# Kernel tuning notes

Measured on AMD Instinct MI355X. Metric: run time of the kernel, lower is better.

The kernel has to match this reference:

```python
import jax, jax.numpy as jnp
import numpy as np

N_LAYERS = 6
C = 768          # hidden_channels
FC = 3072        # filter_channels
H = 12           # n_heads
KC = C // H      # k_channels = 64
KS = 3           # ffn kernel_size
W = 4            # window_size
B = 8
T = 512
EPS = 1e-5


def setup_inputs() -> dict:
    key = jax.random.key(0)
    ks = iter(jax.random.split(key, 24))
    def rn(shape, s=0.02):
        return jax.random.normal(next(ks), shape, dtype=jnp.float32) * s
    inp = {}
    inp['x'] = jax.random.normal(next(ks), (B, C, T), dtype=jnp.float32)
    inp['x_lengths'] = jax.random.randint(next(ks), (B,), T // 2, T + 1, dtype=jnp.int32)
    inp['conv_q_w'] = rn((N_LAYERS, C, C))
    inp['conv_q_b'] = rn((N_LAYERS, C))
    inp['conv_k_w'] = rn((N_LAYERS, C, C))
    inp['conv_k_b'] = rn((N_LAYERS, C))
    inp['conv_v_w'] = rn((N_LAYERS, C, C))
    inp['conv_v_b'] = rn((N_LAYERS, C))
    inp['conv_o_w'] = rn((N_LAYERS, C, C))
    inp['conv_o_b'] = rn((N_LAYERS, C))
    inp['emb_rel_k'] = rn((N_LAYERS, 1, 2 * W + 1, KC), KC ** -0.5)
    inp['emb_rel_v'] = rn((N_LAYERS, 1, 2 * W + 1, KC), KC ** -0.5)
    inp['norm1_g'] = jnp.ones((N_LAYERS, C), jnp.float32)
    inp['norm1_b'] = jnp.zeros((N_LAYERS, C), jnp.float32)
    inp['ffn_w1'] = rn((N_LAYERS, FC, C, KS))
    inp['ffn_b1'] = rn((N_LAYERS, FC))
    inp['ffn_w2'] = rn((N_LAYERS, C, FC, KS))
    inp['ffn_b2'] = rn((N_LAYERS, C))
    inp['norm2_g'] = jnp.ones((N_LAYERS, C), jnp.float32)
    inp['norm2_b'] = jnp.zeros((N_LAYERS, C), jnp.float32)
    return inp


def _layer_norm(x, g, b):
    # x: [B, C, T]; normalize over channel dim (torch code transposes then layer_norms)
    m = jnp.mean(x, axis=1, keepdims=True)
    v = jnp.mean(jnp.square(x - m), axis=1, keepdims=True)
    return (x - m) * jax.lax.rsqrt(v + EPS) * g[None, :, None] + b[None, :, None]


def _conv1d_same(x, w, b):
    # x: [B, Cin, T], w: [Cout, Cin, K], same padding ((K-1)//2, K//2)
    k = w.shape[-1]
    y = jax.lax.conv_general_dilated(x, w, (1,), [((k - 1) // 2, k // 2)],
                                     dimension_numbers=('NCH', 'OIH', 'NCH'))
    return y + b[None, :, None]


def _get_relative_embeddings(emb, length):
    # emb: [1, 2W+1, KC] -> [1, 2*length-1, KC]
    pad_l = max(length - (W + 1), 0)
    start = max(W + 1 - length, 0)
    e = jnp.pad(emb, ((0, 0), (pad_l, pad_l), (0, 0)))
    return e[:, start:start + 2 * length - 1]


def _rel_to_abs(x):
    # x: [B, H, L, 2L-1] -> [B, H, L, L]
    b, h, L, _ = x.shape
    x = jnp.pad(x, ((0, 0), (0, 0), (0, 0), (0, 1)))
    x = x.reshape(b, h, L * 2 * L)
    x = jnp.pad(x, ((0, 0), (0, 0), (0, L - 1)))
    return x.reshape(b, h, L + 1, 2 * L - 1)[:, :, :L, L - 1:]


def _abs_to_rel(x):
    # x: [B, H, L, L] -> [B, H, L, 2L-1]
    b, h, L, _ = x.shape
    x = jnp.pad(x, ((0, 0), (0, 0), (0, 0), (0, L - 1)))
    x = x.reshape(b, h, L * (2 * L - 1))
    x = jnp.pad(x, ((0, 0), (0, 0), (L, 0)))
    return x.reshape(b, h, L, 2 * L)[:, :, :, 1:]


def _encoder(x, x_lengths, conv_q_w, conv_q_b, conv_k_w, conv_k_b, conv_v_w, conv_v_b,
             conv_o_w, conv_o_b, emb_rel_k, emb_rel_v, norm1_g, norm1_b,
             ffn_w1, ffn_b1, ffn_w2, ffn_b2, norm2_g, norm2_b):
    Bn, Cc, Tt = x.shape
    mask = (jnp.arange(Tt)[None, :] < x_lengths[:, None]).astype(x.dtype)[:, None, :]  # [B,1,T]
    attn_mask = mask[:, :, :, None] * mask[:, :, None, :]  # [B,1,T,T]
    x = x * mask
    scale = KC ** -0.5
    for i in range(N_LAYERS):
        xm = x * mask
        q = jnp.einsum('bct,oc->bot', xm, conv_q_w[i]) + conv_q_b[i][None, :, None]
        k = jnp.einsum('bct,oc->bot', xm, conv_k_w[i]) + conv_k_b[i][None, :, None]
        v = jnp.einsum('bct,oc->bot', xm, conv_v_w[i]) + conv_v_b[i][None, :, None]
        # [B, C, T] -> [B, H, T, KC]
        qh = q.reshape(Bn, H, KC, Tt).transpose(0, 1, 3, 2) * scale
        kh = k.reshape(Bn, H, KC, Tt).transpose(0, 1, 3, 2)
        vh = v.reshape(Bn, H, KC, Tt).transpose(0, 1, 3, 2)
        scores = jnp.einsum('bhtd,bhsd->bhts', qh, kh)
        rel_k = _get_relative_embeddings(emb_rel_k[i], Tt)  # [1, 2T-1, KC]
        rel_logits = jnp.einsum('bhtd,rd->bhtr', qh, rel_k[0])
        scores = scores + _rel_to_abs(rel_logits)
        scores = jnp.where(attn_mask == 0, -1e4, scores)
        p = jax.nn.softmax(scores, axis=-1)
        out = jnp.einsum('bhts,bhsd->bhtd', p, vh)
        rel_w = _abs_to_rel(p)  # [B, H, T, 2T-1]
        rel_v = _get_relative_embeddings(emb_rel_v[i], Tt)
        out = out + jnp.einsum('bhtr,rd->bhtd', rel_w, rel_v[0])
        out = out.transpose(0, 1, 3, 2).reshape(Bn, Cc, Tt)
        y = jnp.einsum('bct,oc->bot', out, conv_o_w[i]) + conv_o_b[i][None, :, None]
        x = _layer_norm(x + y, norm1_g[i], norm1_b[i])
        # FFN (relu, non-causal same padding)
        h = jax.nn.relu(_conv1d_same(x * mask, ffn_w1[i], ffn_b1[i]))
        y = _conv1d_same(h * mask, ffn_w2[i], ffn_b2[i]) * mask
        x = _layer_norm(x + y, norm2_g[i], norm2_b[i])
    return x * mask


def reference(x, x_lengths, conv_q_w, conv_q_b, conv_k_w, conv_k_b, conv_v_w, conv_v_b,
              conv_o_w, conv_o_b, emb_rel_k, emb_rel_v, norm1_g, norm1_b,
              ffn_w1, ffn_b1, ffn_w2, ffn_b2, norm2_g, norm2_b):
    return _encoder(x, x_lengths, conv_q_w, conv_q_b, conv_k_w, conv_k_b, conv_v_w, conv_v_b,
                    conv_o_w, conv_o_b, emb_rel_k, emb_rel_v, norm1_g, norm1_b,
                    ffn_w1, ffn_b1, ffn_w2, ffn_b2, norm2_g, norm2_b)
```

## Files before the change

kernel.cpp:

```cpp
#include <hip/hip_runtime.h>

#define DI __device__ __forceinline__

typedef short bf16x8 __attribute__((ext_vector_type(8)));
typedef float f32x4 __attribute__((ext_vector_type(4)));
typedef unsigned short u16;

static DI float bfu2f(unsigned short u) {
    return __uint_as_float(((unsigned)u) << 16);
}
static DI unsigned short f2bu(float f) {
    unsigned u = __float_as_uint(f);
    u += 0x7fffu + ((u >> 16) & 1u);
    return (unsigned short)(u >> 16);
}

static DI void gld16(const u16* g, u16* l) {
    __builtin_amdgcn_global_load_lds(
        (const __attribute__((address_space(1))) void*)g,
        (__attribute__((address_space(3))) void*)l, 16, 0, 0);
}

static DI void swz_block(int& bx, int& by) {
    const int gx = gridDim.x;
    const int n = gx * gridDim.y;
    const int ord = blockIdx.y * gx + blockIdx.x;
    const int cpx = n >> 3;
    const int s = (ord & 7) * cpx + (ord >> 3);
    bx = s % gx;
    by = s / gx;
}

__global__ void zinit(u16* z) { z[threadIdx.x] = 0; }

__global__ __launch_bounds__(256) void cvt_1x1(
    const float* __restrict__ q, const float* __restrict__ k,
    const float* __restrict__ v, const float* __restrict__ o,
    u16* __restrict__ out)
{
    const int sel = blockIdx.y;
    const float* src = (sel == 0) ? q : (sel == 1) ? k : (sel == 2) ? v : o;
    const int i = blockIdx.x * 256 + threadIdx.x;
    const float4 w = ((const float4*)src)[i];
    ushort4 s;
    s.x = f2bu(w.x); s.y = f2bu(w.y); s.z = f2bu(w.z); s.w = f2bu(w.w);
    ((ushort4*)(out + (size_t)sel * 589824))[i] = s;
}

__global__ __launch_bounds__(256) void cvt_k3(
    const float* __restrict__ in, u16* __restrict__ out, int M, int K)
{
    const int i = blockIdx.x * 256 + threadIdx.x;
    const int m = i / (K / 4);
    const int c4 = (i - m * (K / 4)) * 4;
    const float* ap = in + ((size_t)m * K + c4) * 3;
    const float4 w0 = *(const float4*)ap;
    const float4 w1 = *(const float4*)(ap + 4);
    const float4 w2 = *(const float4*)(ap + 8);
    ushort4 s0, s1, s2;
    s0.x = f2bu(w0.x); s0.y = f2bu(w0.w); s0.z = f2bu(w1.z); s0.w = f2bu(w2.y);
    s1.x = f2bu(w0.y); s1.y = f2bu(w1.x); s1.z = f2bu(w1.w); s1.w = f2bu(w2.z);
    s2.x = f2bu(w0.z); s2.y = f2bu(w1.y); s2.z = f2bu(w2.x); s2.w = f2bu(w2.w);
    const size_t PS = (size_t)M * K;
    const size_t off = (size_t)m * K + c4;
    *(ushort4*)(out + off) = s0;
    *(ushort4*)(out + PS + off) = s1;
    *(ushort4*)(out + 2 * PS + off) = s2;
}

template<int BM, int BN, int KS, bool MASK_IN, bool RELU, bool MASK_OUT>
static DI void gemm_dev(const u16* __restrict__ A, size_t PS,
                        const float* __restrict__ bias,
                        const u16* __restrict__ Bin,
                        u16* __restrict__ Cout,
                        const int* __restrict__ lens,
                        const u16* __restrict__ zpage,
                        int K, int ldB, int ldC, int m0, int n0)
{
    constexpr int HALO = (KS == 3) ? 1 : 0;
    constexpr int MI = BM / 32;
    constexpr int NI = BN / 32;
    constexpr int nACH = KS * BM / 8;
    constexpr int nBCH = BN / 8;
    static_assert(nACH % 4 == 0 && nBCH % 4 == 0, "chunks per wave");

    __shared__ __align__(16) u16 As[KS * BM][64];
    __shared__ __align__(16) u16 Bs[BN + 2 * HALO][64];

    const int tid = threadIdx.x;
    const int batch = n0 >> 9;
    const int len0 = lens[batch];
    const int lane = tid & 63;
    const int wid = tid >> 6;
    const int wm = (wid >> 1) * (BM / 2);
    const int wn = (wid & 1) * (BN / 2);
    const int fr = lane & 15;
    const int fg = lane >> 4;
    const int l8 = lane >> 3;
    const int lg = lane & 7;
    const int sga = lg ^ l8;
    const int sgb = lg ^ ((HALO + l8) & 7);

    f32x4 acc[MI][NI];
#pragma unroll
    for (int i = 0; i < MI; ++i)
#pragma unroll
        for (int j = 0; j < NI; ++j) {
            f32x4 z = {0.f, 0.f, 0.f, 0.f};
            acc[i][j] = z;
        }

    for (int c0 = 0; c0 < K; c0 += 64) {
#pragma unroll
        for (int c = 0; c < nACH / 4; ++c) {
            const int ch = c * 4 + wid;
            const int tap = (ch * 8) / BM;
            const int row0 = (ch * 8) & (BM - 1);
            const u16* g = A + (size_t)tap * PS
                             + (size_t)(m0 + row0 + l8) * K + c0 + sga * 8;
            gld16(g, &As[ch * 8][0]);
        }
#pragma unroll
        for (int c = 0; c < nBCH / 4; ++c) {
            const int ch = c * 4 + wid;
            const int gr = n0 + ch * 8 + l8;
            bool v = true;
            if (MASK_IN) v = (gr & 511) < len0;
            const u16* g = v ? (Bin + (size_t)gr * ldB + c0 + sgb * 8)
                             : (zpage + sgb * 8);
            gld16(g, &Bs[HALO + ch * 8][0]);
        }
        if (KS == 3 && tid < 16) {
            const int hs = tid >> 3, j = tid & 7;
            const int rl = hs * (BN + 1);
            const int gr = n0 - 1 + hs * (BN + 1);
            bool v = ((unsigned)gr < 4096u) && ((gr >> 9) == batch);
            if (MASK_IN && v) v = (gr & 511) < len0;
            uint4 q = {0u, 0u, 0u, 0u};
            if (v) q = *(const uint4*)(Bin + (size_t)gr * ldB + c0 + j * 8);
            *(uint4*)&Bs[rl][(j ^ (rl & 7)) * 8] = q;
        }
        __syncthreads();
#pragma unroll
        for (int kh = 0; kh < 2; ++kh) {
            const int kg = kh * 4;
#pragma unroll
            for (int tap = 0; tap < KS; ++tap) {
                bf16x8 af[MI], bgv[NI];
#pragma unroll
                for (int mi = 0; mi < MI; ++mi)
                    af[mi] = *(const bf16x8*)&As[tap * BM + wm + mi * 16 + fr]
                                               [((kg + fg) ^ (fr & 7)) * 8];
#pragma unroll
                for (int ni = 0; ni < NI; ++ni)
                    bgv[ni] = *(const bf16x8*)&Bs[wn + ni * 16 + fr + tap]
                                                [((kg + fg) ^ ((fr + tap) & 7)) * 8];
#pragma unroll
                for (int mi = 0; mi < MI; ++mi)
#pragma unroll
                    for (int ni = 0; ni < NI; ++ni)
                        acc[mi][ni] = __builtin_amdgcn_mfma_f32_16x16x32_bf16(
                            af[mi], bgv[ni], acc[mi][ni], 0, 0, 0);
            }
        }
        __syncthreads();
    }
#pragma unroll
    for (int mi = 0; mi < MI; ++mi) {
        const int m = m0 + wm + mi * 16 + (lane >> 4) * 4;
        const float4 bi = *(const float4*)(bias + m);
#pragma unroll
        for (int ni = 0; ni < NI; ++ni) {
            const int g = n0 + wn + ni * 16 + fr;
            float r0 = acc[mi][ni][0] + bi.x;
            float r1 = acc[mi][ni][1] + bi.y;
            float r2 = acc[mi][ni][2] + bi.z;
            float r3 = acc[mi][ni][3] + bi.w;
            if (RELU) {
                r0 = fmaxf(r0, 0.f); r1 = fmaxf(r1, 0.f);
                r2 = fmaxf(r2, 0.f); r3 = fmaxf(r3, 0.f);
            }
            ushort4 s;
            s.x = f2bu(r0); s.y = f2bu(r1); s.z = f2bu(r2); s.w = f2bu(r3);
            if (MASK_OUT && ((g & 511) >= len0)) { s.x = 0; s.y = 0; s.z = 0; s.w = 0; }
            *(ushort4*)(Cout + (size_t)g * ldC + m) = s;
        }
    }
}

template<int BM, int BN, int KS, bool MASK_IN, bool RELU, bool MASK_OUT>
__global__ __launch_bounds__(256) void mfma_gemm(
    const u16* __restrict__ A, size_t PS, const float* __restrict__ bias,
    const u16* __restrict__ Bin, u16* __restrict__ Cout,
    const int* __restrict__ lens, const u16* __restrict__ zpage,
    int K, int ldB, int ldC)
{
    int bx, by;
    swz_block(bx, by);
    gemm_dev<BM, BN, KS, MASK_IN, RELU, MASK_OUT>(
        A, PS, bias, Bin, Cout, lens, zpage, K, ldB, ldC, by * BM, bx * BN);
}

__global__ __launch_bounds__(256) void mfma_qkv(
    const u16* __restrict__ W,
    const float* __restrict__ qb, const float* __restrict__ kb,
    const float* __restrict__ vb,
    const u16* __restrict__ Xb, u16* __restrict__ QKV,
    const int* __restrict__ lens, const u16* __restrict__ zpage)
{
    int bx, by;
    swz_block(bx, by);
    const int sel = by / 12;
    const int m0 = (by % 12) * 64;
    const u16* A = W + (size_t)sel * 589824;
    const float* bi = (sel == 0) ? qb : (sel == 1) ? kb : vb;
    gemm_dev<64, 128, 1, true, false, false>(
        A, 0, bi, Xb, QKV + sel * 768, lens, zpage, 768, 768, 2304, m0, bx * 128);
}

__global__ __launch_bounds__(256) void transp_v(
    const u16* __restrict__ QKV, u16* __restrict__ Vt)
{
    __shared__ u16 tile[64][65];
    const int tid = threadIdx.x;
    const int bh = blockIdx.y;
    const int b = bh / 12, h = bh - b * 12;
    const int t0 = blockIdx.x * 64;
    const u16* src = QKV + ((size_t)(b * 512 + t0)) * 2304 + 1536 + h * 64;
    const int rr = tid >> 2, c0 = (tid & 3) * 16;
#pragma unroll
    for (int j = 0; j < 4; ++j) {
        const ushort4 v = *(const ushort4*)(src + (size_t)rr * 2304 + c0 + j * 4);
        tile[rr][c0 + j * 4 + 0] = v.x;
        tile[rr][c0 + j * 4 + 1] = v.y;
        tile[rr][c0 + j * 4 + 2] = v.z;
        tile[rr][c0 + j * 4 + 3] = v.w;
    }
    __syncthreads();
    const int d = tid >> 2, tc = (tid & 3) * 16;
    u16* dst = Vt + (size_t)bh * 64 * 512 + (size_t)d * 512 + t0 + tc;
#pragma unroll
    for (int j = 0; j < 4; ++j) {
        ushort4 o;
        o.x = tile[tc + j * 4 + 0][d];
        o.y = tile[tc + j * 4 + 1][d];
        o.z = tile[tc + j * 4 + 2][d];
        o.w = tile[tc + j * 4 + 3][d];
        *(ushort4*)(dst + j * 4) = o;
    }
}

__global__ __launch_bounds__(256, 4) void attn_mfma(
    const u16* __restrict__ QKV, const u16* __restrict__ Vt,
    const float* __restrict__ relk, const float* __restrict__ relv,
    const int* __restrict__ lens, u16* __restrict__ Out)
{
    const int T = 512, H = 12;
    const int tid = threadIdx.x;
    const int t0 = blockIdx.x * 16;
    const int bh = blockIdx.y;
    const int b = bh / H, h = bh - b * H;
    const int len = lens[b];

    __shared__ u16 Qs[16][72];
    __shared__ float S[16][528];
    __shared__ float RB[16][12];
    __shared__ float Lsum[16];

    const int lane = tid & 63;
    const int w = tid >> 6;
    const int fr = lane & 15;
    const int fg = lane >> 4;

    {
        const int qr = tid >> 4, d4 = (tid & 15) * 4;
        const ushort4 q4 = *(const ushort4*)(
            QKV + ((size_t)(b * 512 + t0 + qr)) * 2304 + h * 64 + d4);
        *(ushort4*)&Qs[qr][d4] = q4;
    }
    __syncthreads();

    if (tid < 144) {
        const int rr = tid / 9, o = tid - (tid / 9) * 9;
        float s = 0.f;
        for (int d = 0; d < 64; ++d) s += bfu2f(Qs[rr][d]) * relk[o * 64 + d];
        RB[rr][o] = s;
    }
    __syncthreads();

    {
        bf16x8 qa0 = *(const bf16x8*)&Qs[fr][fg * 8];
        bf16x8 qa1 = *(const bf16x8*)&Qs[fr][32 + fg * 8];
        const u16* Kbase = QKV + ((size_t)(b * 512)) * 2304 + 768 + h * 64;
        f32x4 sa[8];
#pragma unroll
        for (int f = 0; f < 8; ++f) {
            const int s0 = w * 128 + f * 16;
            const u16* kp = Kbase + (size_t)(s0 + fr) * 2304 + fg * 8;
            const bf16x8 kb0 = *(const bf16x8*)kp;
            const bf16x8 kb1 = *(const bf16x8*)(kp + 32);
            f32x4 z = {0.f, 0.f, 0.f, 0.f};
            z = __builtin_amdgcn_mfma_f32_16x16x32_bf16(qa0, kb0, z, 0, 0, 0);
            sa[f] = __builtin_amdgcn_mfma_f32_16x16x32_bf16(qa1, kb1, z, 0, 0, 0);
        }
#pragma unroll
        for (int f = 0; f < 8; ++f) {
            const int s_abs = w * 128 + f * 16 + fr;
#pragma unroll
            for (int i = 0; i < 4; ++i) {
                const int r = fg * 4 + i;
                const int t_abs = t0 + r;
                float v = sa[f][i];
                const int off = s_abs - t_abs;
                if (off >= -4 && off <= 4) v += RB[r][off + 4];
                v *= 0.125f;
                if (s_abs >= len || t_abs >= len) v = -1e4f;
                S[r][s_abs] = v;
            }
        }
    }
    __syncthreads();

    {
        const int r = tid >> 4, lx = tid & 15;
        float sv[32];
        float mx = -3.0e38f;
#pragma unroll
        for (int j = 0; j < 32; ++j) {
            sv[j] = S[r][lx + 16 * j];
            mx = fmaxf(mx, sv[j]);
        }
#pragma unroll
        for (int m = 8; m >= 1; m >>= 1) mx = fmaxf(mx, __shfl_xor(mx, m));
        char* rowp = (char*)&S[0][0] + r * 2112;
        float sum = 0.f;
#pragma unroll
        for (int j = 0; j < 32; ++j) {
            const int c = lx + 16 * j;
            const float p = __expf(sv[j] - mx);
            sum += p;
            const u16 hi = f2bu(p);
            const u16 lo = f2bu(p - bfu2f(hi));
            *(u16*)(rowp + c * 2) = hi;
            *(u16*)(rowp + 1056 + c * 2) = lo;
        }
#pragma unroll
        for (int m = 8; m >= 1; m >>= 1) sum += __shfl_xor(sum, m);
        if (lx == 0) Lsum[r] = sum;
    }
    __syncthreads();

    f32x4 oacc = {0.f, 0.f, 0.f, 0.f};
    {
        const u16* vtp = Vt + (size_t)bh * 64 * 512 + (size_t)(w * 16 + fr) * 512;
        const char* prow = (const char*)&S[0][0] + fr * 2112;
#pragma unroll 4
        for (int ks = 0; ks < 16; ++ks) {
            const int k0 = ks * 32;
            const bf16x8 pa_hi = *(const bf16x8*)(prow + (k0 + fg * 8) * 2);
            const bf16x8 pa_lo = *(const bf16x8*)(prow + 1056 + (k0 + fg * 8) * 2);
            const bf16x8 vb = *(const bf16x8*)(vtp + k0 + fg * 8);
            oacc = __builtin_amdgcn_mfma_f32_16x16x32_bf16(pa_hi, vb, oacc, 0, 0, 0);
            oacc = __builtin_amdgcn_mfma_f32_16x16x32_bf16(pa_lo, vb, oacc, 0, 0, 0);
        }
    }

    {
        const int d = w * 16 + fr;
        float rvv[9];
#pragma unroll
        for (int o = 0; o < 9; ++o) rvv[o] = relv[o * 64 + d];
        const char* Sbase = (const char*)&S[0][0];
#pragma unroll
        for (int i = 0; i < 4; ++i) {
            const int r = fg * 4 + i;
            const int t_abs = t0 + r;
            float o = oacc[i];
            const char* rp = Sbase + r * 2112;
#pragma unroll
            for (int dd = 0; dd < 9; ++dd) {
                const int s = t_abs + dd - 4;
                if (s >= 0 && s < T) {
                    const float p = bfu2f(*(const u16*)(rp + s * 2))
                                  + bfu2f(*(const u16*)(rp + 1056 + s * 2));
                    o += p * rvv[dd];
                }
            }
            o *= 1.0f / Lsum[r];
            Out[((size_t)(b * 512 + t_abs)) * 768 + h * 64 + d] = f2bu(o);
        }
    }
}

__global__ __launch_bounds__(256) void ln_kernel(
    float* __restrict__ X, const u16* __restrict__ Y,
    const float* __restrict__ g, const float* __restrict__ bb,
    u16* __restrict__ Xb)
{
    const int row = blockIdx.x * 4 + (threadIdx.x >> 6);
    const int lane = threadIdx.x & 63;
    float* xp = X + (size_t)row * 768;
    const u16* yp = Y + (size_t)row * 768;
    u16* xbp = Xb + (size_t)row * 768;
    float v[12];
    float s1 = 0.f, s2 = 0.f;
#pragma unroll
    for (int j = 0; j < 3; ++j) {
        const int c = lane * 4 + j * 256;
        const float4 x4 = *(const float4*)(xp + c);
        const ushort4 y4 = *(const ushort4*)(yp + c);
        const float a0 = x4.x + bfu2f(y4.x);
        const float a1 = x4.y + bfu2f(y4.y);
        const float a2 = x4.z + bfu2f(y4.z);
        const float a3 = x4.w + bfu2f(y4.w);
        v[j * 4 + 0] = a0; v[j * 4 + 1] = a1; v[j * 4 + 2] = a2; v[j * 4 + 3] = a3;
        s1 += a0 + a1 + a2 + a3;
        s2 += a0 * a0 + a1 * a1 + a2 * a2 + a3 * a3;
    }
#pragma unroll
    for (int m = 32; m >= 1; m >>= 1) {
        s1 += __shfl_xor(s1, m);
        s2 += __shfl_xor(s2, m);
    }
    const float mean = s1 * (1.0f / 768.0f);
    const float rstd = rsqrtf(s2 * (1.0f / 768.0f) - mean * mean + 1e-5f);
#pragma unroll
    for (int j = 0; j < 3; ++j) {
        const int c = lane * 4 + j * 256;
        const float4 g4 = *(const float4*)(g + c);
        const float4 b4 = *(const float4*)(bb + c);
        float4 o;
        o.x = (v[j * 4 + 0] - mean) * rstd * g4.x + b4.x;
        o.y = (v[j * 4 + 1] - mean) * rstd * g4.y + b4.y;
        o.z = (v[j * 4 + 2] - mean) * rstd * g4.z + b4.z;
        o.w = (v[j * 4 + 3] - mean) * rstd * g4.w + b4.w;
        *(float4*)(xp + c) = o;
        ushort4 s;
        s.x = f2bu(o.x); s.y = f2bu(o.y); s.z = f2bu(o.z); s.w = f2bu(o.w);
        *(ushort4*)(xbp + c) = s;
    }
}

__global__ __launch_bounds__(256) void transpose_in(
    const float* __restrict__ in, float* __restrict__ X, u16* __restrict__ Xb)
{
    __shared__ float tile[32][33];
    const int b = blockIdx.z;
    const int t0 = blockIdx.x * 32, c0 = blockIdx.y * 32;
    const int lx = threadIdx.x & 31, ly = threadIdx.x >> 5;
    const float* ip = in + ((size_t)b * 768 + c0) * 512 + t0;
#pragma unroll
    for (int j = 0; j < 4; ++j)
        tile[ly + j * 8][lx] = ip[(size_t)(ly + j * 8) * 512 + lx];
    __syncthreads();
    float* xp = X + ((size_t)b * 512 + t0) * 768 + c0;
    u16* xbp = Xb + ((size_t)b * 512 + t0) * 768 + c0;
#pragma unroll
    for (int j = 0; j < 4; ++j) {
        const float val = tile[lx][ly + j * 8];
        xp[(size_t)(ly + j * 8) * 768 + lx] = val;
        xbp[(size_t)(ly + j * 8) * 768 + lx] = f2bu(val);
    }
}

__global__ __launch_bounds__(256) void finalize_kernel(
    const float* __restrict__ X, const int* __restrict__ lens,
    float* __restrict__ out)
{
    __shared__ float tile[32][33];
    const int b = blockIdx.z;
    const int t0 = blockIdx.x * 32, c0 = blockIdx.y * 32;
    const int lx = threadIdx.x & 31, ly = threadIdx.x >> 5;
    const float* xp = X + ((size_t)b * 512 + t0) * 768 + c0;
#pragma unroll
    for (int j = 0; j < 4; ++j)
        tile[ly + j * 8][lx] = xp[(size_t)(ly + j * 8) * 768 + lx];
    __syncthreads();
    const int len = lens[b];
    float* op = out + ((size_t)b * 768 + c0) * 512 + t0;
    const bool on = (t0 + lx) < len;
#pragma unroll
    for (int j = 0; j < 4; ++j)
        op[(size_t)(ly + j * 8) * 512 + lx] = on ? tile[lx][ly + j * 8] : 0.0f;
}

extern "C" void kernel_launch(void* const* d_in, const int* in_sizes, int n_in,
                              void* d_out, int out_size, void* d_ws, size_t ws_size,
                              hipStream_t stream)
{
    (void)in_sizes; (void)n_in; (void)out_size; (void)ws_size;
    const int C = 768, FC = 3072, NL = 6;
    const size_t NROW = (size_t)8 * 512;

    const float* xin  = (const float*)d_in[0];
    const int*   lens = (const int*)d_in[1];
    const float* qw = (const float*)d_in[2];
    const float* qb = (const float*)d_in[3];
    const float* kw = (const float*)d_in[4];
    const float* kb = (const float*)d_in[5];
    const float* vw = (const float*)d_in[6];
    const float* vb = (const float*)d_in[7];
    const float* ow = (const float*)d_in[8];
    const float* ob = (const float*)d_in[9];
    const float* rk = (const float*)d_in[10];
    const float* rv = (const float*)d_in[11];
    const float* n1g = (const float*)d_in[12];
    const float* n1b = (const float*)d_in[13];
    const float* w1 = (const float*)d_in[14];
    const float* b1 = (const float*)d_in[15];
    const float* w2 = (const float*)d_in[16];
    const float* b2 = (const float*)d_in[17];
    const float* n2g = (const float*)d_in[18];
    const float* n2b = (const float*)d_in[19];

    char* p0 = (char*)d_ws;
    float* X = (float*)p0;
    u16* QKV = (u16*)(p0 + NROW * 768 * 4);
    u16* ATb = QKV + NROW * 2304;
    u16* Yb  = ATb + NROW * 768;
    u16* Xb  = Yb + NROW * 768;
    u16* Wc  = Xb + NROW * 768;
    u16* zp  = Wc + (size_t)3 * FC * C;
    u16* Hb  = QKV;
    u16* Vt  = Yb;

    zinit<<<dim3(1), 64, 0, stream>>>(zp);
    transpose_in<<<dim3(16, 24, 8), 256, 0, stream>>>(xin, X, Xb);

    for (int i = 0; i < NL; ++i) {
        cvt_1x1<<<dim3(576, 4), 256, 0, stream>>>(
            qw + (size_t)i * C * C, kw + (size_t)i * C * C,
            vw + (size_t)i * C * C, ow + (size_t)i * C * C, Wc);
        mfma_qkv<<<dim3(32, 36), 256, 0, stream>>>(
            Wc, qb + i * C, kb + i * C, vb + i * C, Xb, QKV, lens, zp);
        transp_v<<<dim3(8, 96), 256, 0, stream>>>(QKV, Vt);
        attn_mfma<<<dim3(32, 96), 256, 0, stream>>>(
            QKV, Vt, rk + (size_t)i * 9 * 64, rv + (size_t)i * 9 * 64, lens, ATb);
        mfma_gemm<64, 64, 1, false, false, false><<<dim3(64, 12), 256, 0, stream>>>(
            Wc + (size_t)3 * 589824, 0, ob + i * C, ATb, Yb, lens, zp, 768, 768, 768);
        ln_kernel<<<dim3(1024), 256, 0, stream>>>(X, Yb, n1g + i * C, n1b + i * C, Xb);
        cvt_k3<<<dim3(2304), 256, 0, stream>>>(
            w1 + (size_t)i * FC * C * 3, Wc, FC, C);
        mfma_gemm<64, 128, 3, true, true, true><<<dim3(32, 48), 256, 0, stream>>>(
            Wc, (size_t)FC * C, b1 + i * FC, Xb, Hb, lens, zp, 768, 768, 3072);
        cvt_k3<<<dim3(2304), 256, 0, stream>>>(
            w2 + (size_t)i * C * FC * 3, Wc, C, FC);
        mfma_gemm<64, 64, 3, false, false, true><<<dim3(64, 12), 256, 0, stream>>>(
            Wc, (size_t)C * FC, b2 + i * C, Hb, Yb, lens, zp, 3072, 3072, 768);
        ln_kernel<<<dim3(1024), 256, 0, stream>>>(X, Yb, n2g + i * C, n2b + i * C, Xb);
    }

    finalize_kernel<<<dim3(16, 24, 8), 256, 0, stream>>>(X, lens, (float*)d_out);
}
```

Baseline: 1.929 ms.

## Double-buffer GEMM LDS staging and write V transposed from GEMM epilogue

Adds an optional double-buffered shared-memory pipeline to the MFMA GEMM, so the async global-to-LDS load of the next K tile overlaps compute on the current one. It is enabled for the QKV, output-projection and second FFN GEMMs, but not for the first FFN GEMM. The halo rows for the k=3 conv are now fetched with async global_load_lds into extra rows instead of synchronous loads. V is split into its own GEMM that writes the transposed layout directly, which removes the separate transpose kernel. Double buffering doubles LDS use and may lower occupancy, and the transposed V stores are scattered 2-byte writes.

```diff
diff --git a/kernel.cpp b/kernel.cpp
--- a/kernel.cpp
+++ b/kernel.cpp
@@ -68,7 +68,8 @@
     *(ushort4*)(out + 2 * PS + off) = s2;
 }
 
-template<int BM, int BN, int KS, bool MASK_IN, bool RELU, bool MASK_OUT>
+template<int BM, int BN, int KS, bool MASK_IN, bool RELU, bool MASK_OUT,
+         bool VT_OUT, int DB>
 static DI void gemm_dev(const u16* __restrict__ A, size_t PS,
                         const float* __restrict__ bias,
                         const u16* __restrict__ Bin,
@@ -78,14 +79,15 @@
                         int K, int ldB, int ldC, int m0, int n0)
 {
     constexpr int HALO = (KS == 3) ? 1 : 0;
+    constexpr int BROWS = (KS == 3) ? BN + 8 : BN;
     constexpr int MI = BM / 32;
     constexpr int NI = BN / 32;
     constexpr int nACH = KS * BM / 8;
     constexpr int nBCH = BN / 8;
     static_assert(nACH % 4 == 0 && nBCH % 4 == 0, "chunks per wave");
 
-    __shared__ __align__(16) u16 As[KS * BM][64];
-    __shared__ __align__(16) u16 Bs[BN + 2 * HALO][64];
+    __shared__ __align__(16) u16 As[DB + 1][KS * BM][64];
+    __shared__ __align__(16) u16 Bs[DB + 1][BROWS][64];
 
     const int tid = threadIdx.x;
     const int batch = n0 >> 9;
@@ -99,7 +101,6 @@
     const int l8 = lane >> 3;
     const int lg = lane & 7;
     const int sga = lg ^ l8;
-    const int sgb = lg ^ ((HALO + l8) & 7);
 
     f32x4 acc[MI][NI];
 #pragma unroll
@@ -110,7 +111,7 @@
             acc[i][j] = z;
         }
 
-    for (int c0 = 0; c0 < K; c0 += 64) {
+    auto stage = [&](int buf, int c0) {
 #pragma unroll
         for (int c = 0; c < nACH / 4; ++c) {
             const int ch = c * 4 + wid;
@@ -118,7 +119,7 @@
             const int row0 = (ch * 8) & (BM - 1);
             const u16* g = A + (size_t)tap * PS
                              + (size_t)(m0 + row0 + l8) * K + c0 + sga * 8;
-            gld16(g, &As[ch * 8][0]);
+            gld16(g, &As[buf][ch * 8][0]);
         }
 #pragma unroll
         for (int c = 0; c < nBCH / 4; ++c) {
@@ -126,21 +127,36 @@
             const int gr = n0 + ch * 8 + l8;
             bool v = true;
             if (MASK_IN) v = (gr & 511) < len0;
-            const u16* g = v ? (Bin + (size_t)gr * ldB + c0 + sgb * 8)
-                             : (zpage + sgb * 8);
-            gld16(g, &Bs[HALO + ch * 8][0]);
-        }
-        if (KS == 3 && tid < 16) {
-            const int hs = tid >> 3, j = tid & 7;
-            const int rl = hs * (BN + 1);
-            const int gr = n0 - 1 + hs * (BN + 1);
-            bool v = ((unsigned)gr < 4096u) && ((gr >> 9) == batch);
-            if (MASK_IN && v) v = (gr & 511) < len0;
-            uint4 q = {0u, 0u, 0u, 0u};
-            if (v) q = *(const uint4*)(Bin + (size_t)gr * ldB + c0 + j * 8);
-            *(uint4*)&Bs[rl][(j ^ (rl & 7)) * 8] = q;
-        }
-        __syncthreads();
+            const u16* g = v ? (Bin + (size_t)gr * ldB + c0 + sga * 8)
+                             : (zpage + sga * 8);
+            gld16(g, &Bs[buf][ch * 8][0]);
+        }
+        if constexpr (KS == 3) {
+            if (wid == 3) {
+                const u16* g;
+                if (l8 == 0) {
+                    const int gr = n0 - 1;
+                    bool v = (gr >= 0) && ((gr >> 9) == batch);
+                    if (MASK_IN && v) v = (gr & 511) < len0;
+                    const int sg = lg ^ (BN & 7);
+                    g = v ? (Bin + (size_t)gr * ldB + c0 + sg * 8)
+                          : (zpage + sg * 8);
+                } else if (l8 == 1) {
+                    const int gr = n0 + BN;
+                    bool v = (gr < 4096) && ((gr >> 9) == batch);
+                    if (MASK_IN && v) v = (gr & 511) < len0;
+                    const int sg = lg ^ ((BN + 1) & 7);
+                    g = v ? (Bin + (size_t)gr * ldB + c0 + sg * 8)
+                          : (zpage + sg * 8);
+                } else {
+                    g = zpage + lg * 8;
+                }
+                gld16(g, &Bs[buf][BN][0]);
+            }
+        }
+    };
+
+    auto compute = [&](int buf) {
 #pragma unroll
         for (int kh = 0; kh < 2; ++kh) {
             const int kg = kh * 4;
@@ -149,12 +165,17 @@
                 bf16x8 af[MI], bgv[NI];
 #pragma unroll
                 for (int mi = 0; mi < MI; ++mi)
-                    af[mi] = *(const bf16x8*)&As[tap * BM + wm + mi * 16 + fr]
+                    af[mi] = *(const bf16x8*)&As[buf][tap * BM + wm + mi * 16 + fr]
                                                [((kg + fg) ^ (fr & 7)) * 8];
 #pragma unroll
-                for (int ni = 0; ni < NI; ++ni)
-                    bgv[ni] = *(const bf16x8*)&Bs[wn + ni * 16 + fr + tap]
-                                                [((kg + fg) ^ ((fr + tap) & 7)) * 8];
+                for (int ni = 0; ni < NI; ++ni) {
+                    const int ar = wn + ni * 16 + fr + tap - HALO;
+                    int lr = ar;
+                    if constexpr (KS == 3)
+                        lr = (ar < 0) ? BN : ((ar >= BN) ? BN + 1 : ar);
+                    bgv[ni] = *(const bf16x8*)&Bs[buf][lr]
+                                                [((kg + fg) ^ (lr & 7)) * 8];
+                }
 #pragma unroll
                 for (int mi = 0; mi < MI; ++mi)
 #pragma unroll
@@ -163,8 +184,27 @@
                             af[mi], bgv[ni], acc[mi][ni], 0, 0, 0);
             }
         }
+    };
+
+    if constexpr (DB == 1) {
+        stage(0, 0);
         __syncthreads();
-    }
+        int cur = 0;
+        for (int c0 = 0; c0 < K; c0 += 64) {
+            if (c0 + 64 < K) stage(cur ^ 1, c0 + 64);
+            compute(cur);
+            __syncthreads();
+            cur ^= 1;
+        }
+    } else {
+        for (int c0 = 0; c0 < K; c0 += 64) {
+            stage(0, c0);
+            __syncthreads();
+            compute(0);
+            __syncthreads();
+        }
+    }
+
 #pragma unroll
     for (int mi = 0; mi < MI; ++mi) {
         const int m = m0 + wm + mi * 16 + (lane >> 4) * 4;
@@ -180,15 +220,26 @@
                 r0 = fmaxf(r0, 0.f); r1 = fmaxf(r1, 0.f);
                 r2 = fmaxf(r2, 0.f); r3 = fmaxf(r3, 0.f);
             }
-            ushort4 s;
-            s.x = f2bu(r0); s.y = f2bu(r1); s.z = f2bu(r2); s.w = f2bu(r3);
-            if (MASK_OUT && ((g & 511) >= len0)) { s.x = 0; s.y = 0; s.z = 0; s.w = 0; }
-            *(ushort4*)(Cout + (size_t)g * ldC + m) = s;
-        }
-    }
-}
-
-template<int BM, int BN, int KS, bool MASK_IN, bool RELU, bool MASK_OUT>
+            if constexpr (VT_OUT) {
+                u16* vt = Cout + (((size_t)(batch * 12 + (m >> 6)) * 64
+                                   + (m & 63)) * 512) + (g & 511);
+                vt[0 * 512] = f2bu(r0);
+                vt[1 * 512] = f2bu(r1);
+                vt[2 * 512] = f2bu(r2);
+                vt[3 * 512] = f2bu(r3);
+            } else {
+                ushort4 s;
+                s.x = f2bu(r0); s.y = f2bu(r1); s.z = f2bu(r2); s.w = f2bu(r3);
+                if (MASK_OUT && ((g & 511) >= len0)) {
+                    s.x = 0; s.y = 0; s.z = 0; s.w = 0;
+                }
+                *(ushort4*)(Cout + (size_t)g * ldC + m) = s;
+            }
+        }
+    }
+}
+
+template<int BM, int BN, int KS, bool MASK_IN, bool RELU, bool MASK_OUT, int DB>
 __global__ __launch_bounds__(256) void mfma_gemm(
     const u16* __restrict__ A, size_t PS, const float* __restrict__ bias,
     const u16* __restrict__ Bin, u16* __restrict__ Cout,
@@ -197,14 +248,13 @@
 {
     int bx, by;
     swz_block(bx, by);
-    gemm_dev<BM, BN, KS, MASK_IN, RELU, MASK_OUT>(
+    gemm_dev<BM, BN, KS, MASK_IN, RELU, MASK_OUT, false, DB>(
         A, PS, bias, Bin, Cout, lens, zpage, K, ldB, ldC, by * BM, bx * BN);
 }
 
 __global__ __launch_bounds__(256) void mfma_qkv(
     const u16* __restrict__ W,
     const float* __restrict__ qb, const float* __restrict__ kb,
-    const float* __restrict__ vb,
     const u16* __restrict__ Xb, u16* __restrict__ QKV,
     const int* __restrict__ lens, const u16* __restrict__ zpage)
 {
@@ -213,41 +263,22 @@
     const int sel = by / 12;
     const int m0 = (by % 12) * 64;
     const u16* A = W + (size_t)sel * 589824;
-    const float* bi = (sel == 0) ? qb : (sel == 1) ? kb : vb;
-    gemm_dev<64, 128, 1, true, false, false>(
-        A, 0, bi, Xb, QKV + sel * 768, lens, zpage, 768, 768, 2304, m0, bx * 128);
-}
-
-__global__ __launch_bounds__(256) void transp_v(
-    const u16* __restrict__ QKV, u16* __restrict__ Vt)
-{
-    __shared__ u16 tile[64][65];
-    const int tid = threadIdx.x;
-    const int bh = blockIdx.y;
-    const int b = bh / 12, h = bh - b * 12;
-    const int t0 = blockIdx.x * 64;
-    const u16* src = QKV + ((size_t)(b * 512 + t0)) * 2304 + 1536 + h * 64;
-    const int rr = tid >> 2, c0 = (tid & 3) * 16;
-#pragma unroll
-    for (int j = 0; j < 4; ++j) {
-        const ushort4 v = *(const ushort4*)(src + (size_t)rr * 2304 + c0 + j * 4);
-        tile[rr][c0 + j * 4 + 0] = v.x;
-        tile[rr][c0 + j * 4 + 1] = v.y;
-        tile[rr][c0 + j * 4 + 2] = v.z;
-        tile[rr][c0 + j * 4 + 3] = v.w;
-    }
-    __syncthreads();
-    const int d = tid >> 2, tc = (tid & 3) * 16;
-    u16* dst = Vt + (size_t)bh * 64 * 512 + (size_t)d * 512 + t0 + tc;
-#pragma unroll
-    for (int j = 0; j < 4; ++j) {
-        ushort4 o;
-        o.x = tile[tc + j * 4 + 0][d];
-        o.y = tile[tc + j * 4 + 1][d];
-        o.z = tile[tc + j * 4 + 2][d];
-        o.w = tile[tc + j * 4 + 3][d];
-        *(ushort4*)(dst + j * 4) = o;
-    }
+    const float* bi = (sel == 0) ? qb : kb;
+    gemm_dev<64, 128, 1, true, false, false, false, 1>(
+        A, 0, bi, Xb, QKV + sel * 768, lens, zpage, 768, 768, 2304,
+        m0, bx * 128);
+}
+
+__global__ __launch_bounds__(256) void mfma_v(
+    const u16* __restrict__ W, const float* __restrict__ vb,
+    const u16* __restrict__ Xb, u16* __restrict__ Vt,
+    const int* __restrict__ lens, const u16* __restrict__ zpage)
+{
+    int bx, by;
+    swz_block(bx, by);
+    gemm_dev<64, 128, 1, true, false, false, true, 1>(
+        W + (size_t)2 * 589824, 0, vb, Xb, Vt, lens, zpage, 768, 768, 0,
+        by * 64, bx * 128);
 }
 
 __global__ __launch_bounds__(256, 4) void attn_mfma(
@@ -531,21 +562,22 @@
         cvt_1x1<<<dim3(576, 4), 256, 0, stream>>>(
             qw + (size_t)i * C * C, kw + (size_t)i * C * C,
             vw + (size_t)i * C * C, ow + (size_t)i * C * C, Wc);
-        mfma_qkv<<<dim3(32, 36), 256, 0, stream>>>(
-            Wc, qb + i * C, kb + i * C, vb + i * C, Xb, QKV, lens, zp);
-        transp_v<<<dim3(8, 96), 256, 0, stream>>>(QKV, Vt);
+        mfma_qkv<<<dim3(32, 24), 256, 0, stream>>>(
+            Wc, qb + i * C, kb + i * C, Xb, QKV, lens, zp);
+        mfma_v<<<dim3(32, 12), 256, 0, stream>>>(
+            Wc, vb + i * C, Xb, Vt, lens, zp);
         attn_mfma<<<dim3(32, 96), 256, 0, stream>>>(
             QKV, Vt, rk + (size_t)i * 9 * 64, rv + (size_t)i * 9 * 64, lens, ATb);
-        mfma_gemm<64, 64, 1, false, false, false><<<dim3(64, 12), 256, 0, stream>>>(
+        mfma_gemm<64, 64, 1, false, false, false, 1><<<dim3(64, 12), 256, 0, stream>>>(
             Wc + (size_t)3 * 589824, 0, ob + i * C, ATb, Yb, lens, zp, 768, 768, 768);
         ln_kernel<<<dim3(1024), 256, 0, stream>>>(X, Yb, n1g + i * C, n1b + i * C, Xb);
         cvt_k3<<<dim3(2304), 256, 0, stream>>>(
             w1 + (size_t)i * FC * C * 3, Wc, FC, C);
-        mfma_gemm<64, 128, 3, true, true, true><<<dim3(32, 48), 256, 0, stream>>>(
+        mfma_gemm<64, 128, 3, true, true, true, 0><<<dim3(32, 48), 256, 0, stream>>>(
             Wc, (size_t)FC * C, b1 + i * FC, Xb, Hb, lens, zp, 768, 768, 3072);
         cvt_k3<<<dim3(2304), 256, 0, stream>>>(
             w2 + (size_t)i * C * FC * 3, Wc, C, FC);
-        mfma_gemm<64, 64, 3, false, false, true><<<dim3(64, 12), 256, 0, stream>>>(
+        mfma_gemm<64, 64, 3, false, false, true, 1><<<dim3(64, 12), 256, 0, stream>>>(
             Wc, (size_t)C * FC, b2 + i * C, Hb, Yb, lens, zp, 3072, 3072, 768);
         ln_kernel<<<dim3(1024), 256, 0, stream>>>(X, Yb, n2g + i * C, n2b + i * C, Xb);
     }
```

New measurement: 2.135 ms. 1.11x slower.
